# Kernel tuning notes

Measured on AMD Instinct MI355X. Metric: run time of the kernel, lower is better.

The kernel has to match this reference:

```python
import jax, jax.numpy as jnp
import numpy as np

S, B, E, H, V = 512, 128, 1024, 1024, 50257

def setup_inputs() -> dict:
    key = jax.random.key(0)
    ks = jax.random.split(key, 6)
    scale = 1.0 / np.sqrt(H)
    return {
        "X": jax.random.randint(ks[0], (S, B), 0, V),
        "embd_weight": jax.random.normal(ks[1], (V, E), dtype=jnp.float32),
        "W_ih": jax.random.uniform(ks[2], (4 * H, E), minval=-scale, maxval=scale, dtype=jnp.float32),
        "W_hh": jax.random.uniform(ks[3], (4 * H, H), minval=-scale, maxval=scale, dtype=jnp.float32),
        "b_ih": jax.random.uniform(ks[4], (4 * H,), minval=-scale, maxval=scale, dtype=jnp.float32),
        "b_hh": jax.random.uniform(ks[5], (4 * H,), minval=-scale, maxval=scale, dtype=jnp.float32),
    }

def reference(X, embd_weight, W_ih, W_hh, b_ih, b_hh):
    # X: [S, B] int indices -> embedded [S, B, E]
    emb = embd_weight[X]
    b = b_ih + b_hh  # [4H]
    Bsz = X.shape[1]
    h0 = jnp.zeros((Bsz, H), dtype=emb.dtype)
    c0 = jnp.zeros((Bsz, H), dtype=emb.dtype)

    def step(carry, xt):
        h, c = carry
        # PyTorch LSTM gate order: i, f, g, o
        gates = xt @ W_ih.T + h @ W_hh.T + b  # [B, 4H]
        i, f, g, o = jnp.split(gates, 4, axis=-1)
        c_new = jax.nn.sigmoid(f) * c + jax.nn.sigmoid(i) * jnp.tanh(g)
        h_new = jax.nn.sigmoid(o) * jnp.tanh(c_new)
        return (h_new, c_new), None

    (h_last, _), _ = jax.lax.scan(step, (h0, c0), emb)
    yt = h_last[None]  # [1, B, H] — output of last timestep
    # Faithful to source: LogSoftmax(dim=1) normalizes over the BATCH axis
    return jax.nn.log_softmax(yt, axis=1)
```

## Files before the change

### kernel.cpp

```cpp
#include <hip/hip_runtime.h>
#include <cstdint>
#include <cstddef>

#define SEQ   512
#define BATCH 128
#define EMB   1024
#define HID   1024
#define VOCAB 50257
#define GATES 4096

typedef _Float16 f16x8 __attribute__((ext_vector_type(8)));
typedef float    f32x4 __attribute__((ext_vector_type(4)));
typedef unsigned short u16;
typedef u16 u16x8 __attribute__((ext_vector_type(8)));

__device__ inline u16 f2h(float x) { union { _Float16 h; u16 u; } c; c.h = (_Float16)x; return c.u; }
__device__ inline float h2f(u16 u) { union { u16 u; _Float16 h; } c; c.u = u; return (float)c.h; }

__global__ void cast_f32_f16_kernel(const float* __restrict__ src, u16* __restrict__ dst, int n4) {
  int i = blockIdx.x * blockDim.x + threadIdx.x;
  int stride = gridDim.x * blockDim.x;
  for (; i < n4; i += stride) {
    float4 v = ((const float4*)src)[i];
    ushort4 o;
    o.x = f2h(v.x); o.y = f2h(v.y); o.z = f2h(v.z); o.w = f2h(v.w);
    ((ushort4*)dst)[i] = o;
  }
}

__global__ void init_kernel(const float* __restrict__ bih, const float* __restrict__ bhh,
                            float* __restrict__ bias, u16* __restrict__ h0, int* __restrict__ sync) {
  int i = blockIdx.x * blockDim.x + threadIdx.x;
  if (i < GATES) bias[i] = bih[i] + bhh[i];
  ushort4 z; z.x = z.y = z.z = z.w = 0;
  ((ushort4*)h0)[i] = z;
  if (i < 8192) sync[i] = 0;
}

__global__ __launch_bounds__(256, 1) void fused_kernel(
    const u16* __restrict__ embw, const u16* __restrict__ wih,
    const u16* __restrict__ whh, const float* __restrict__ bias,
    const int* __restrict__ X, u16* __restrict__ gx,
    u16* __restrict__ hring, float* __restrict__ hlast,
    float* __restrict__ out, int* __restrict__ flags, int Tc)
{
  extern __shared__ u16 LdsRaw[];
  const int tid = threadIdx.x;
  const int w = tid >> 6, lane = tid & 63;
  int* gxcnt = flags + 4096;

  if (blockIdx.x >= 128) {
    u16* Als = LdsRaw;
    u16* Bls = LdsRaw + 4096;
    const int ewg = blockIdx.x - 128;
    const int wm = w & 1, wn = w >> 1;
    const u16* afp = Als + (lane >> 4) * 1024 + (wm * 64 + (lane & 15)) * 8;
    const u16* bfp = Bls + (lane >> 4) * 1024 + (wn * 64 + (lane & 15)) * 8;
    int skq[4], srow[4], shalf[4];
#pragma unroll
    for (int s = 0; s < 4; ++s) {
      const int idx = s * 256 + tid;
      shalf[s] = idx >> 9; skq[s] = (idx >> 7) & 3; srow[s] = idx & 127;
    }
    for (int tile = ewg; tile < SEQ * 32; tile += 128) {
      const int T = tile >> 5;
      const int colbase = (tile & 31) << 7;
      if (T >= Tc) {
        const int need = T - Tc + 1;
        for (;;) {
          int f = __hip_atomic_load(flags + (tid & 127) * 32,
                                    __ATOMIC_RELAXED, __HIP_MEMORY_SCOPE_AGENT);
          if (__syncthreads_and(f >= need)) break;
          __builtin_amdgcn_s_sleep(8);
        }
      }
      size_t sg[4];
#pragma unroll
      for (int s = 0; s < 4; ++s) {
        if (shalf[s] == 0) sg[s] = (size_t)X[(size_t)T * BATCH + srow[s]] * EMB + skq[s] * 8;
        else               sg[s] = (size_t)(colbase + srow[s]) * EMB + skq[s] * 8;
      }
      f32x4 acc[4][4] = {};
      u16x8 vq[4][4];
#pragma unroll
      for (int d = 0; d < 4; ++d)
#pragma unroll
        for (int s = 0; s < 4; ++s)
          vq[d][s] = *(const u16x8*)((shalf[s] ? wih : embw) + sg[s] + d * 32);
      for (int kb = 0; kb < 32; kb += 4) {
#pragma unroll
        for (int d = 0; d < 4; ++d) {
#pragma unroll
          for (int s = 0; s < 4; ++s)
            *(u16x8*)((shalf[s] ? Bls : Als) + skq[s] * 1024 + srow[s] * 8) = vq[d][s];
          __syncthreads();
          if (kb + d + 4 < 32) {
#pragma unroll
            for (int s = 0; s < 4; ++s)
              vq[d][s] = *(const u16x8*)((shalf[s] ? wih : embw) + sg[s] + (kb + d + 4) * 32);
          }
          f16x8 af[4], bf[4];
#pragma unroll
          for (int mt = 0; mt < 4; ++mt) af[mt] = *(const f16x8*)(afp + mt * 128);
#pragma unroll
          for (int nt = 0; nt < 4; ++nt) bf[nt] = *(const f16x8*)(bfp + nt * 128);
#pragma unroll
          for (int mt = 0; mt < 4; ++mt)
#pragma unroll
            for (int nt = 0; nt < 4; ++nt)
              acc[mt][nt] = __builtin_amdgcn_mfma_f32_16x16x32_f16(af[mt], bf[nt], acc[mt][nt], 0, 0, 0);
          __syncthreads();
        }
      }
      const size_t outbase = (size_t)(T % Tc) * ((size_t)GATES * BATCH);
#pragma unroll
      for (int mt = 0; mt < 4; ++mt) {
#pragma unroll
        for (int nt = 0; nt < 4; ++nt) {
          const int n  = colbase + wn * 64 + nt * 16 + (lane & 15);
          const int b0 = wm * 64 + mt * 16 + ((lane >> 4) << 2);
#pragma unroll
          for (int p = 0; p < 4; ++p)
            __hip_atomic_store(gx + outbase + (size_t)(b0 + p) * GATES + n,
                               f2h(acc[mt][nt][p]),
                               __ATOMIC_RELAXED, __HIP_MEMORY_SCOPE_AGENT);
        }
      }
      asm volatile("s_waitcnt vmcnt(0)" ::: "memory");
      __syncthreads();
      if (tid == 0)
        __hip_atomic_fetch_add(gxcnt + T, 1, __ATOMIC_RELAXED, __HIP_MEMORY_SCOPE_AGENT);
    }
    return;
  }

  f32x4* Red = (f32x4*)LdsRaw;
  const int jloc = lane & 15, lq = lane >> 4;
  const int bh = blockIdx.x & 1;
  const int jw = blockIdx.x >> 1;

  f16x8 wreg[4][8];
#pragma unroll
  for (int g = 0; g < 4; ++g)
#pragma unroll
    for (int ks = 0; ks < 8; ++ks)
      wreg[g][ks] = *(const f16x8*)(whh + ((size_t)g * HID + jw * 16 + jloc) * HID
                                          + w * 256 + ks * 32 + lq * 8);

  const int b  = bh * 64 + w * 16 + jloc;
  const int j0 = jw * 16 + lq * 4;
  f32x4 bs[4];
#pragma unroll
  for (int g = 0; g < 4; ++g) bs[g] = *(const f32x4*)(bias + g * HID + j0);

  f32x4 cc; cc[0] = cc[1] = cc[2] = cc[3] = 0.f;

  const u16* hb = hring + (size_t)(w * 32 + lq) * 1024 + (size_t)(bh * 64 + jloc) * 8;
  const int hw_idx = (jw * 2 + (lq >> 1)) * 1024 + b * 8 + (lq & 1) * 4;
  const u16* gbase = gx + (size_t)b * GATES + j0;
  const int* fpoll = flags + ((w * 16 + (lane & 15)) * 2 + bh) * 32;

  int slot = 0;
  unsigned long long vXu[4];
  {
    const int* cnt = gxcnt;
    for (;;) {
      int c = __hip_atomic_load(cnt, __ATOMIC_RELAXED, __HIP_MEMORY_SCOPE_AGENT);
      if (c >= 32) break;
      __builtin_amdgcn_s_sleep(1);
    }
    asm volatile("" ::: "memory");
#pragma unroll
    for (int g = 0; g < 4; ++g)
      vXu[g] = __hip_atomic_load((const unsigned long long*)(gbase + g * 1024),
                                 __ATOMIC_RELAXED, __HIP_MEMORY_SCOPE_AGENT);
  }

  for (int t = 0; t < SEQ; ++t) {
    if (t > 0) {
      for (;;) {
        int a = __hip_atomic_load(fpoll, __ATOMIC_RELAXED, __HIP_MEMORY_SCOPE_AGENT);
        if (__all(a >= t)) break;
        __builtin_amdgcn_s_sleep(1);
      }
      asm volatile("" ::: "memory");
      __builtin_amdgcn_sched_barrier(0);
    }
    const u16* ap = hb + (size_t)t * (BATCH * HID);
    f16x8 av[8][4];
#pragma unroll
    for (int ks = 0; ks < 8; ++ks)
#pragma unroll
      for (int nt = 0; nt < 4; ++nt)
        av[ks][nt] = *(const f16x8*)(ap + ks * 4096 + nt * 128);
    __builtin_amdgcn_sched_barrier(0);
    f32x4 acc[4][4] = {};
#pragma unroll
    for (int ks = 0; ks < 8; ++ks)
#pragma unroll
      for (int g = 0; g < 4; ++g)
#pragma unroll
        for (int nt = 0; nt < 4; ++nt)
          acc[g][nt] = __builtin_amdgcn_mfma_f32_16x16x32_f16(wreg[g][ks], av[ks][nt], acc[g][nt], 0, 0, 0);
#pragma unroll
    for (int g = 0; g < 4; ++g)
#pragma unroll
      for (int nt = 0; nt < 4; ++nt)
        if (nt != w) Red[((w * 4 + g) * 4 + nt) * 64 + lane] = acc[g][nt];
    __syncthreads();
    f32x4 gate[4];
#pragma unroll
    for (int g = 0; g < 4; ++g) {
      gate[g] = acc[g][w];
#pragma unroll
      for (int wp = 0; wp < 4; ++wp)
        if (wp != w) gate[g] += Red[((wp * 4 + g) * 4 + w) * 64 + lane];
    }
    u16* hout = hring + (size_t)(t + 1) * (BATCH * HID);
    float hn4[4];
#pragma unroll
    for (int p = 0; p < 4; ++p) {
      float gi = gate[0][p] + h2f((u16)(vXu[0] >> (16 * p))) + bs[0][p];
      float gf = gate[1][p] + h2f((u16)(vXu[1] >> (16 * p))) + bs[1][p];
      float gg = gate[2][p] + h2f((u16)(vXu[2] >> (16 * p))) + bs[2][p];
      float go = gate[3][p] + h2f((u16)(vXu[3] >> (16 * p))) + bs[3][p];
      float ii = 1.f / (1.f + __expf(-gi));
      float ff = 1.f / (1.f + __expf(-gf));
      float e2 = __expf(-2.f * fabsf(gg));
      float tg = copysignf((1.f - e2) / (1.f + e2), gg);
      float oo = 1.f / (1.f + __expf(-go));
      float cn = ff * cc[p] + ii * tg;
      cc[p] = cn;
      float e2c = __expf(-2.f * fabsf(cn));
      float tc = copysignf((1.f - e2c) / (1.f + e2c), cn);
      hn4[p] = oo * tc;
    }
    unsigned long long hp = (unsigned long long)f2h(hn4[0])
                          | ((unsigned long long)f2h(hn4[1]) << 16)
                          | ((unsigned long long)f2h(hn4[2]) << 32)
                          | ((unsigned long long)f2h(hn4[3]) << 48);
    __hip_atomic_store((unsigned long long*)(hout + hw_idx), hp,
                       __ATOMIC_RELAXED, __HIP_MEMORY_SCOPE_AGENT);
    if (t + 1 == SEQ) {
      union { float f[2]; unsigned long long u; } pk;
      pk.f[0] = hn4[0]; pk.f[1] = hn4[1];
      __hip_atomic_store((unsigned long long*)(hlast + (size_t)b * HID + j0), pk.u,
                         __ATOMIC_RELAXED, __HIP_MEMORY_SCOPE_AGENT);
      pk.f[0] = hn4[2]; pk.f[1] = hn4[3];
      __hip_atomic_store((unsigned long long*)(hlast + (size_t)b * HID + j0 + 2), pk.u,
                         __ATOMIC_RELAXED, __HIP_MEMORY_SCOPE_AGENT);
    }
    asm volatile("s_waitcnt vmcnt(0)" ::: "memory");
    __builtin_amdgcn_sched_barrier(0);
    __builtin_amdgcn_s_barrier();
    if (tid == 0)
      __hip_atomic_store(flags + blockIdx.x * 32, t + 1,
                         __ATOMIC_RELAXED, __HIP_MEMORY_SCOPE_AGENT);
    if (t + 1 < SEQ) {
      slot = (slot + 1 == Tc) ? 0 : slot + 1;
      const int* cnt = gxcnt + (t + 1);
      for (;;) {
        int c = __hip_atomic_load(cnt, __ATOMIC_RELAXED, __HIP_MEMORY_SCOPE_AGENT);
        if (c >= 32) break;
        __builtin_amdgcn_s_sleep(1);
      }
      asm volatile("" ::: "memory");
      __builtin_amdgcn_sched_barrier(0);
      const u16* gslot = gbase + (size_t)slot * ((size_t)GATES * BATCH);
#pragma unroll
      for (int g = 0; g < 4; ++g)
        vXu[g] = __hip_atomic_load((const unsigned long long*)(gslot + g * 1024),
                                   __ATOMIC_RELAXED, __HIP_MEMORY_SCOPE_AGENT);
    }
  }

  if (blockIdx.x < 4) {
    for (;;) {
      int f = __hip_atomic_load(flags + (tid & 127) * 32,
                                __ATOMIC_RELAXED, __HIP_MEMORY_SCOPE_AGENT);
      if (__syncthreads_and(f >= SEQ)) break;
      __builtin_amdgcn_s_sleep(4);
    }
    const int j = blockIdx.x * 256 + tid;
    float m = -1e30f;
    for (int b2 = 0; b2 < BATCH; ++b2) m = fmaxf(m, hlast[(size_t)b2 * HID + j]);
    float s = 0.f;
    for (int b2 = 0; b2 < BATCH; ++b2) s += expf(hlast[(size_t)b2 * HID + j] - m);
    const float lse = m + logf(s);
    for (int b2 = 0; b2 < BATCH; ++b2)
      out[(size_t)b2 * HID + j] = hlast[(size_t)b2 * HID + j] - lse;
  }
}

extern "C" void kernel_launch(void* const* d_in, const int* in_sizes, int n_in,
                              void* d_out, int out_size, void* d_ws, size_t ws_size,
                              hipStream_t stream) {
  const int*   X    = (const int*)d_in[0];
  const float* embd = (const float*)d_in[1];
  const float* wih  = (const float*)d_in[2];
  const float* whh  = (const float*)d_in[3];
  const float* bih  = (const float*)d_in[4];
  const float* bhh  = (const float*)d_in[5];
  float* out = (float*)d_out;

  char* p = (char*)d_ws;
  auto alloc = [&](size_t bytes) { char* r = p; p += (bytes + 255) & ~(size_t)255; return r; };
  u16*   embw    = (u16*)alloc((size_t)VOCAB * EMB * 2);
  u16*   wihh    = (u16*)alloc((size_t)GATES * EMB * 2);
  u16*   whhh    = (u16*)alloc((size_t)GATES * HID * 2);
  float* bias    = (float*)alloc((size_t)GATES * 4);
  u16*   hring   = (u16*)alloc((size_t)(SEQ + 1) * BATCH * HID * 2);
  float* hlast   = (float*)alloc((size_t)BATCH * HID * 4);
  int*   flags   = (int*)alloc(32768);
  size_t used = (size_t)(p - (char*)d_ws);
  size_t avail = ws_size > used ? ws_size - used : 0;
  long long Tc = (long long)(avail / ((size_t)GATES * BATCH * 2));
  if (Tc > SEQ) Tc = SEQ;
  if (Tc < 1) return;
  u16* gx = (u16*)alloc((size_t)Tc * GATES * BATCH * 2);
  int Tci = (int)Tc;

  hipFuncSetAttribute((const void*)fused_kernel, hipFuncAttributeMaxDynamicSharedMemorySize, 98304);

  cast_f32_f16_kernel<<<2048, 256, 0, stream>>>(embd, embw, VOCAB * EMB / 4);
  cast_f32_f16_kernel<<<256, 256, 0, stream>>>(wih, wihh, GATES * EMB / 4);
  cast_f32_f16_kernel<<<256, 256, 0, stream>>>(whh, whhh, GATES * HID / 4);
  init_kernel<<<128, 256, 0, stream>>>(bih, bhh, bias, hring, flags);

  fused_kernel<<<dim3(256), dim3(256), 98304, stream>>>(
      embw, wihh, whhh, bias, X, gx, hring, hlast, out, flags, Tci);
}
```

Measured before the change: 4.012 ms.

## Replace per-step flag polling with poisoned h-ring data polling and double-buffer gx

The h ring is pre-filled with a NaN sentinel so each recurrent block spins directly on the hidden-state data it needs, instead of polling producer flags and then issuing a separate load. The per-step vmcnt wait before the flag store is dropped. Input-projection gates are prefetched two steps ahead into alternating register sets, hiding the gx counter wait. The cost is an extra kernel that writes the whole h ring (about 128 MB), plus the risk that a legitimate fp16 value matching the sentinel, or a partially visible 16-byte read, breaks correctness.

```diff
diff --git a/kernel.cpp b/kernel.cpp
--- a/kernel.cpp
+++ b/kernel.cpp
@@ -16,6 +16,8 @@
 
 __device__ inline u16 f2h(float x) { union { _Float16 h; u16 u; } c; c.h = (_Float16)x; return c.u; }
 __device__ inline float h2f(u16 u) { union { u16 u; _Float16 h; } c; c.u = u; return (float)c.h; }
+
+#define HPOISON 0x7FFFull
 
 __global__ void cast_f32_f16_kernel(const float* __restrict__ src, u16* __restrict__ dst, int n4) {
   int i = blockIdx.x * blockDim.x + threadIdx.x;
@@ -35,6 +37,15 @@
   ushort4 z; z.x = z.y = z.z = z.w = 0;
   ((ushort4*)h0)[i] = z;
   if (i < 8192) sync[i] = 0;
+}
+
+__global__ void poison_kernel(u16* __restrict__ hring) {
+  const size_t n16 = (size_t)SEQ * BATCH * HID / 8;
+  size_t i = (size_t)blockIdx.x * blockDim.x + threadIdx.x;
+  const size_t stride = (size_t)gridDim.x * blockDim.x;
+  uint4* base = (uint4*)(hring + (size_t)BATCH * HID);
+  uint4 pv; pv.x = pv.y = pv.z = pv.w = 0x7FFF7FFFu;
+  for (; i < n16; i += stride) base[i] = pv;
 }
 
 __global__ __launch_bounds__(256, 1) void fused_kernel(
@@ -158,50 +169,65 @@
   const u16* hb = hring + (size_t)(w * 32 + lq) * 1024 + (size_t)(bh * 64 + jloc) * 8;
   const int hw_idx = (jw * 2 + (lq >> 1)) * 1024 + b * 8 + (lq & 1) * 4;
   const u16* gbase = gx + (size_t)b * GATES + j0;
-  const int* fpoll = flags + ((w * 16 + (lane & 15)) * 2 + bh) * 32;
-
-  int slot = 0;
-  unsigned long long vXu[4];
+
+  unsigned long long vA0, vA1, vA2, vA3, vB0, vB1, vB2, vB3;
   {
-    const int* cnt = gxcnt;
     for (;;) {
-      int c = __hip_atomic_load(cnt, __ATOMIC_RELAXED, __HIP_MEMORY_SCOPE_AGENT);
+      int c = __hip_atomic_load(gxcnt + 0, __ATOMIC_RELAXED, __HIP_MEMORY_SCOPE_AGENT);
       if (c >= 32) break;
       __builtin_amdgcn_s_sleep(1);
     }
-    asm volatile("" ::: "memory");
-#pragma unroll
-    for (int g = 0; g < 4; ++g)
-      vXu[g] = __hip_atomic_load((const unsigned long long*)(gbase + g * 1024),
-                                 __ATOMIC_RELAXED, __HIP_MEMORY_SCOPE_AGENT);
-  }
+    vA0 = __hip_atomic_load((const unsigned long long*)(gbase + 0 * 1024), __ATOMIC_RELAXED, __HIP_MEMORY_SCOPE_AGENT);
+    vA1 = __hip_atomic_load((const unsigned long long*)(gbase + 1 * 1024), __ATOMIC_RELAXED, __HIP_MEMORY_SCOPE_AGENT);
+    vA2 = __hip_atomic_load((const unsigned long long*)(gbase + 2 * 1024), __ATOMIC_RELAXED, __HIP_MEMORY_SCOPE_AGENT);
+    vA3 = __hip_atomic_load((const unsigned long long*)(gbase + 3 * 1024), __ATOMIC_RELAXED, __HIP_MEMORY_SCOPE_AGENT);
+    for (;;) {
+      int c = __hip_atomic_load(gxcnt + 1, __ATOMIC_RELAXED, __HIP_MEMORY_SCOPE_AGENT);
+      if (c >= 32) break;
+      __builtin_amdgcn_s_sleep(1);
+    }
+    const u16* g1 = gbase + (size_t)GATES * BATCH;
+    vB0 = __hip_atomic_load((const unsigned long long*)(g1 + 0 * 1024), __ATOMIC_RELAXED, __HIP_MEMORY_SCOPE_AGENT);
+    vB1 = __hip_atomic_load((const unsigned long long*)(g1 + 1 * 1024), __ATOMIC_RELAXED, __HIP_MEMORY_SCOPE_AGENT);
+    vB2 = __hip_atomic_load((const unsigned long long*)(g1 + 2 * 1024), __ATOMIC_RELAXED, __HIP_MEMORY_SCOPE_AGENT);
+    vB3 = __hip_atomic_load((const unsigned long long*)(g1 + 3 * 1024), __ATOMIC_RELAXED, __HIP_MEMORY_SCOPE_AGENT);
+  }
+  int snext = 2;
+
+  union HV { unsigned long long q[2]; f16x8 v; };
 
   for (int t = 0; t < SEQ; ++t) {
-    if (t > 0) {
-      for (;;) {
-        int a = __hip_atomic_load(fpoll, __ATOMIC_RELAXED, __HIP_MEMORY_SCOPE_AGENT);
-        if (__all(a >= t)) break;
-        __builtin_amdgcn_s_sleep(1);
-      }
-      asm volatile("" ::: "memory");
-      __builtin_amdgcn_sched_barrier(0);
-    }
     const u16* ap = hb + (size_t)t * (BATCH * HID);
-    f16x8 av[8][4];
+    HV hvv[8][4];
+    for (;;) {
+      int bad = 0;
+#pragma unroll
+      for (int ks = 0; ks < 8; ++ks)
+#pragma unroll
+        for (int nt = 0; nt < 4; ++nt) {
+          const unsigned long long* src = (const unsigned long long*)(ap + ks * 4096 + nt * 128);
+          hvv[ks][nt].q[0] = __hip_atomic_load(src,     __ATOMIC_RELAXED, __HIP_MEMORY_SCOPE_AGENT);
+          hvv[ks][nt].q[1] = __hip_atomic_load(src + 1, __ATOMIC_RELAXED, __HIP_MEMORY_SCOPE_AGENT);
+        }
+#pragma unroll
+      for (int ks = 0; ks < 8; ++ks)
+#pragma unroll
+        for (int nt = 0; nt < 4; ++nt)
+          bad |= (int)((hvv[ks][nt].q[0] & 0xFFFFull) == HPOISON)
+               | (int)((hvv[ks][nt].q[1] & 0xFFFFull) == HPOISON);
+      if (!__any(bad)) break;
+    }
+    f32x4 acc[4][4] = {};
 #pragma unroll
     for (int ks = 0; ks < 8; ++ks)
 #pragma unroll
-      for (int nt = 0; nt < 4; ++nt)
-        av[ks][nt] = *(const f16x8*)(ap + ks * 4096 + nt * 128);
-    __builtin_amdgcn_sched_barrier(0);
-    f32x4 acc[4][4] = {};
-#pragma unroll
-    for (int ks = 0; ks < 8; ++ks)
-#pragma unroll
       for (int g = 0; g < 4; ++g)
 #pragma unroll
         for (int nt = 0; nt < 4; ++nt)
-          acc[g][nt] = __builtin_amdgcn_mfma_f32_16x16x32_f16(wreg[g][ks], av[ks][nt], acc[g][nt], 0, 0, 0);
+          acc[g][nt] = __builtin_amdgcn_mfma_f32_16x16x32_f16(wreg[g][ks], hvv[ks][nt].v, acc[g][nt], 0, 0, 0);
+    int gxc = 32;
+    if (t + 2 < SEQ)
+      gxc = __hip_atomic_load(gxcnt + (t + 2), __ATOMIC_RELAXED, __HIP_MEMORY_SCOPE_AGENT);
 #pragma unroll
     for (int g = 0; g < 4; ++g)
 #pragma unroll
@@ -216,14 +242,17 @@
       for (int wp = 0; wp < 4; ++wp)
         if (wp != w) gate[g] += Red[((wp * 4 + g) * 4 + w) * 64 + lane];
     }
+    unsigned long long x0, x1, x2, x3;
+    if (t & 1) { x0 = vB0; x1 = vB1; x2 = vB2; x3 = vB3; }
+    else       { x0 = vA0; x1 = vA1; x2 = vA2; x3 = vA3; }
     u16* hout = hring + (size_t)(t + 1) * (BATCH * HID);
     float hn4[4];
 #pragma unroll
     for (int p = 0; p < 4; ++p) {
-      float gi = gate[0][p] + h2f((u16)(vXu[0] >> (16 * p))) + bs[0][p];
-      float gf = gate[1][p] + h2f((u16)(vXu[1] >> (16 * p))) + bs[1][p];
-      float gg = gate[2][p] + h2f((u16)(vXu[2] >> (16 * p))) + bs[2][p];
-      float go = gate[3][p] + h2f((u16)(vXu[3] >> (16 * p))) + bs[3][p];
+      float gi = gate[0][p] + h2f((u16)(x0 >> (16 * p))) + bs[0][p];
+      float gf = gate[1][p] + h2f((u16)(x1 >> (16 * p))) + bs[1][p];
+      float gg = gate[2][p] + h2f((u16)(x2 >> (16 * p))) + bs[2][p];
+      float go = gate[3][p] + h2f((u16)(x3 >> (16 * p))) + bs[3][p];
       float ii = 1.f / (1.f + __expf(-gi));
       float ff = 1.f / (1.f + __expf(-gf));
       float e2 = __expf(-2.f * fabsf(gg));
@@ -250,29 +279,39 @@
       __hip_atomic_store((unsigned long long*)(hlast + (size_t)b * HID + j0 + 2), pk.u,
                          __ATOMIC_RELAXED, __HIP_MEMORY_SCOPE_AGENT);
     }
-    asm volatile("s_waitcnt vmcnt(0)" ::: "memory");
-    __builtin_amdgcn_sched_barrier(0);
     __builtin_amdgcn_s_barrier();
-    if (tid == 0)
+    if (tid == 0 && t + 1 < SEQ)
       __hip_atomic_store(flags + blockIdx.x * 32, t + 1,
                          __ATOMIC_RELAXED, __HIP_MEMORY_SCOPE_AGENT);
-    if (t + 1 < SEQ) {
-      slot = (slot + 1 == Tc) ? 0 : slot + 1;
-      const int* cnt = gxcnt + (t + 1);
-      for (;;) {
-        int c = __hip_atomic_load(cnt, __ATOMIC_RELAXED, __HIP_MEMORY_SCOPE_AGENT);
-        if (c >= 32) break;
-        __builtin_amdgcn_s_sleep(1);
-      }
-      asm volatile("" ::: "memory");
-      __builtin_amdgcn_sched_barrier(0);
-      const u16* gslot = gbase + (size_t)slot * ((size_t)GATES * BATCH);
-#pragma unroll
-      for (int g = 0; g < 4; ++g)
-        vXu[g] = __hip_atomic_load((const unsigned long long*)(gslot + g * 1024),
-                                   __ATOMIC_RELAXED, __HIP_MEMORY_SCOPE_AGENT);
-    }
-  }
+    if (t + 2 < SEQ) {
+      if (gxc < 32) {
+        const int* cnt = gxcnt + (t + 2);
+        for (;;) {
+          int c = __hip_atomic_load(cnt, __ATOMIC_RELAXED, __HIP_MEMORY_SCOPE_AGENT);
+          if (c >= 32) break;
+          __builtin_amdgcn_s_sleep(1);
+        }
+      }
+      const u16* gs = gbase + (size_t)snext * ((size_t)GATES * BATCH);
+      if (t & 1) {
+        vB0 = __hip_atomic_load((const unsigned long long*)(gs + 0 * 1024), __ATOMIC_RELAXED, __HIP_MEMORY_SCOPE_AGENT);
+        vB1 = __hip_atomic_load((const unsigned long long*)(gs + 1 * 1024), __ATOMIC_RELAXED, __HIP_MEMORY_SCOPE_AGENT);
+        vB2 = __hip_atomic_load((const unsigned long long*)(gs + 2 * 1024), __ATOMIC_RELAXED, __HIP_MEMORY_SCOPE_AGENT);
+        vB3 = __hip_atomic_load((const unsigned long long*)(gs + 3 * 1024), __ATOMIC_RELAXED, __HIP_MEMORY_SCOPE_AGENT);
+      } else {
+        vA0 = __hip_atomic_load((const unsigned long long*)(gs + 0 * 1024), __ATOMIC_RELAXED, __HIP_MEMORY_SCOPE_AGENT);
+        vA1 = __hip_atomic_load((const unsigned long long*)(gs + 1 * 1024), __ATOMIC_RELAXED, __HIP_MEMORY_SCOPE_AGENT);
+        vA2 = __hip_atomic_load((const unsigned long long*)(gs + 2 * 1024), __ATOMIC_RELAXED, __HIP_MEMORY_SCOPE_AGENT);
+        vA3 = __hip_atomic_load((const unsigned long long*)(gs + 3 * 1024), __ATOMIC_RELAXED, __HIP_MEMORY_SCOPE_AGENT);
+      }
+      snext = (snext + 1 == Tc) ? 0 : snext + 1;
+    }
+  }
+  asm volatile("s_waitcnt vmcnt(0)" ::: "memory");
+  __builtin_amdgcn_s_barrier();
+  if (tid == 0)
+    __hip_atomic_store(flags + blockIdx.x * 32, SEQ,
+                       __ATOMIC_RELAXED, __HIP_MEMORY_SCOPE_AGENT);
 
   if (blockIdx.x < 4) {
     for (;;) {
@@ -316,7 +355,7 @@
   size_t avail = ws_size > used ? ws_size - used : 0;
   long long Tc = (long long)(avail / ((size_t)GATES * BATCH * 2));
   if (Tc > SEQ) Tc = SEQ;
-  if (Tc < 1) return;
+  if (Tc < 8) return;
   u16* gx = (u16*)alloc((size_t)Tc * GATES * BATCH * 2);
   int Tci = (int)Tc;
 
@@ -326,6 +365,7 @@
   cast_f32_f16_kernel<<<256, 256, 0, stream>>>(wih, wihh, GATES * EMB / 4);
   cast_f32_f16_kernel<<<256, 256, 0, stream>>>(whh, whhh, GATES * HID / 4);
   init_kernel<<<128, 256, 0, stream>>>(bih, bhh, bias, hring, flags);
+  poison_kernel<<<4096, 256, 0, stream>>>(hring);
 
   fused_kernel<<<dim3(256), dim3(256), 98304, stream>>>(
       embw, wihh, whhh, bias, X, gx, hring, hlast, out, flags, Tci);
```

Result: slower. 4.306 ms (+7.3%).
